# Kernel tuning notes

Hardware: AMD Instinct MI355X
Metric: run time of the kernel (lower is better)

The kernel has to match this reference:

```python
import jax, jax.numpy as jnp
import numpy as np

N = 256          # HiPPO order
DT = 1.0 / 4096  # discretization step ~ 1/L
L, BATCH = 4096, 64
GBT_ALPHA = 0.5  # bilinear transform (matches discretization=0.5)


def _legt_matrices(n):
    # Closed-form HiPPO-LegT transition matrices (Gu et al.), lambda_n=1.
    q = np.arange(n, dtype=np.float64)
    r = (2.0 * q + 1.0) ** 0.5
    j, i = np.meshgrid(q, q)  # i: row index n, j: col index k
    A = -(r[:, None] * np.where(i < j, (-1.0) ** (i - j), 1.0) * r[None, :])
    B = r[:, None]  # (N, 1)
    return A, B


def _discretize_gbt(A, B, dt, alpha):
    # Generalized bilinear transform, identical to scipy cont2discrete('gbt').
    n = A.shape[0]
    I = np.eye(n)
    M = np.linalg.inv(I - dt * alpha * A)
    dA = M @ (I + dt * (1.0 - alpha) * A)
    dB = (M @ (dt * B)).squeeze(-1)
    return dA.astype(np.float32), dB.astype(np.float32)


def setup_inputs() -> dict:
    key = jax.random.key(0)
    A, B = _legt_matrices(N)
    dA, dB = _discretize_gbt(A, B, DT, GBT_ALPHA)
    inputs = jax.random.normal(key, (L, BATCH), dtype=jnp.float32)
    return {"inputs": inputs, "dA": jnp.asarray(dA), "dB": jnp.asarray(dB)}


def reference(inputs, dA, dB):
    # inputs: (L, B); dA: (N, N); dB: (N,)
    # u_t = inputs_t[..., None] * dB  -> (L, B, N)
    u = inputs[..., None] * dB

    def step(c, u_t):
        # c_t = dA @ c_{t-1} + u_t  (row-vector form: c @ dA^T)
        c = c @ dA.T + u_t
        return c, c

    c0 = jnp.zeros(u.shape[1:], dtype=u.dtype)  # (B, N)
    _, cs = jax.lax.scan(step, c0, u)
    return cs  # (L, B, N)
```

## Files before the change

### kernel.cpp

```cpp
#include <hip/hip_runtime.h>
#include <hip/hip_bf16.h>
#include <stdint.h>


#define N 256
#define LSEQ 4096
#define BATCH 64
#define TCH 64
#define NCH 64

using bf16x8 = __attribute__((ext_vector_type(8))) __bf16;
using f32x4  = __attribute__((ext_vector_type(4))) float;

__device__ __forceinline__ unsigned short f2bf(float f) {
  uint32_t x = __builtin_bit_cast(uint32_t, f);
  uint32_t r = x + 0x7fffu + ((x >> 16) & 1u);
  return (unsigned short)(r >> 16);
}
__device__ __forceinline__ float bf2f(unsigned short h) {
  uint32_t x = ((uint32_t)h) << 16;
  return __builtin_bit_cast(float, x);
}

__device__ __forceinline__ int swz(int r, int c) { return r * 32 + ((c ^ ((r >> 1) & 3)) << 3); }

#define OFF_Phi 16777216
#define OFF_Plo 25165824
#define OFF_Kf  33554432
#define OFF_Khi 33619968
#define OFF_Klo 33652736
#define OFF_shi 33685504
#define OFF_slo 35782656
#define OFF_G0  37879808
#define OFF_uT  42074112
#define OFF_Sqh 43122688
#define OFF_Sql 43778048


__device__ __forceinline__ void mm64_tile(const float* __restrict__ A, const float* __restrict__ B,
                                          float* __restrict__ Cw, unsigned short* __restrict__ Chi,
                                          unsigned short* __restrict__ Clo, int bx, int tid,
                                          char* smem) {
  float (*At)[68] = (float(*)[68])smem;
  float (*Bs)[68] = (float(*)[68])(smem + 4352);
  int gr0 = (bx >> 2) * 64, gc0 = (bx & 3) * 64;
  int ty = tid >> 4, tx = tid & 15;
  float acc[4][4];
  #pragma unroll
  for (int r = 0; r < 4; ++r)
    #pragma unroll
    for (int c = 0; c < 4; ++c) acc[r][c] = 0.f;
  int ra = tid >> 2, ka4 = (tid & 3) << 2;
  int kb = tid >> 4, cb4 = (tid & 15) << 2;
  for (int k0 = 0; k0 < 256; k0 += 16) {
    float4 va = *(const float4*)&A[(size_t)(gr0 + ra) * 256 + k0 + ka4];
    At[ka4 + 0][ra] = va.x; At[ka4 + 1][ra] = va.y;
    At[ka4 + 2][ra] = va.z; At[ka4 + 3][ra] = va.w;
    *(float4*)&Bs[kb][cb4] = *(const float4*)&B[(size_t)(k0 + kb) * 256 + gc0 + cb4];
    __syncthreads();
    #pragma unroll
    for (int kk = 0; kk < 16; ++kk) {
      float4 a4 = *(const float4*)&At[kk][ty << 2];
      float4 b4 = *(const float4*)&Bs[kk][tx << 2];
      acc[0][0] += a4.x * b4.x; acc[0][1] += a4.x * b4.y; acc[0][2] += a4.x * b4.z; acc[0][3] += a4.x * b4.w;
      acc[1][0] += a4.y * b4.x; acc[1][1] += a4.y * b4.y; acc[1][2] += a4.y * b4.z; acc[1][3] += a4.y * b4.w;
      acc[2][0] += a4.z * b4.x; acc[2][1] += a4.z * b4.y; acc[2][2] += a4.z * b4.z; acc[2][3] += a4.z * b4.w;
      acc[3][0] += a4.w * b4.x; acc[3][1] += a4.w * b4.y; acc[3][2] += a4.w * b4.z; acc[3][3] += a4.w * b4.w;
    }
    __syncthreads();
  }
  #pragma unroll
  for (int r = 0; r < 4; ++r)
    #pragma unroll
    for (int c = 0; c < 4; ++c) {
      size_t idx = (size_t)(gr0 + ty * 4 + r) * 256 + gc0 + tx * 4 + c;
      float v = acc[r][c];
      Cw[idx] = v;
      unsigned short h = f2bf(v);
      Chi[idx] = h;
      Clo[idx] = f2bf(v - bf2f(h));
    }
}

__device__ __forceinline__ void makeK_part(const float* __restrict__ Pw, const float* __restrict__ dB,
                                           float* __restrict__ Kf, unsigned short* __restrict__ Khi,
                                           unsigned short* __restrict__ Klo, int p, int quarter, int tid) {
  if (p == 0) {
    if (quarter == 0) {
      float v = dB[tid];
      Kf[tid] = v;
      unsigned short h = f2bf(v);
      Khi[tid] = h;
      Klo[tid] = f2bf(v - bf2f(h));
    }
    return;
  }
  int lane = tid & 63, w = tid >> 6;
  const float* M = Pw + (size_t)(p - 1) * 65536;
  float d0 = dB[lane], d1 = dB[lane + 64], d2 = dB[lane + 128], d3 = dB[lane + 192];
  for (int ii = 0; ii < 16; ++ii) {
    int i = quarter * 64 + w * 16 + ii;
    const float* row = M + (size_t)i * 256;
    float acc = row[lane] * d0 + row[lane + 64] * d1 + row[lane + 128] * d2 + row[lane + 192] * d3;
    #pragma unroll
    for (int off = 32; off; off >>= 1) acc += __shfl_xor(acc, off, 64);
    if (lane == 0) {
      Kf[p * 256 + i] = acc;
      unsigned short h = f2bf(acc);
      Khi[p * 256 + i] = h;
      Klo[p * 256 + i] = f2bf(acc - bf2f(h));
    }
  }
}

__device__ __forceinline__ void finals_one(const float* __restrict__ Kf, const float* __restrict__ u,
                                           float* __restrict__ G0, int k, int b, int i) {
  float acc = 0.f;
  int ubase = (k * TCH + 63) * BATCH + b;
  #pragma unroll 8
  for (int p = 0; p < TCH; ++p)
    acc += Kf[p * N + i] * u[ubase - p * BATCH];
  G0[(size_t)(k * BATCH + b) * N + i] = acc;
}

template <int FINAL>
__device__ __forceinline__ void ks_tile(int bx, int tid, const float* __restrict__ Gin,
                                        float* __restrict__ Gout,
                                        const unsigned short* __restrict__ Mh,
                                        const unsigned short* __restrict__ Ml, int shift,
                                        unsigned short* __restrict__ shi,
                                        unsigned short* __restrict__ slo, char* smem) {
  unsigned short* Ah = (unsigned short*)smem;
  unsigned short* Al = (unsigned short*)(smem + 4096);
  unsigned short* Bh = (unsigned short*)(smem + 8192);
  unsigned short* Bl = (unsigned short*)(smem + 12288);
  int kb0 = (bx >> 2) * 64, i0 = (bx & 3) * 64;
  int lane = tid & 63, wid = tid >> 6;
  int wr = wid >> 1, wc = wid & 1;
  int rg = lane >> 4, cl = lane & 15;

  f32x4 acc[2][2];
  #pragma unroll
  for (int mf = 0; mf < 2; ++mf) {
    int m0 = kb0 + wr * 32 + mf * 16 + rg * 4;
    #pragma unroll
    for (int nf = 0; nf < 2; ++nf) {
      int i = i0 + wc * 32 + nf * 16 + cl;
      #pragma unroll
      for (int r = 0; r < 4; ++r)
        acc[mf][nf][r] = Gin[(size_t)(m0 + r) * 256 + i];
    }
  }

  int sr = tid >> 2, kc = tid & 3;
  int sw = swz(sr, kc);
  for (int kt = 0; kt < 8; ++kt) {
    int srow = kb0 + sr - shift;
    if (srow >= 0) {
      const float* src = &Gin[(size_t)srow * 256 + kt * 32 + kc * 8];
      float4 v0 = *(const float4*)src;
      float4 v1 = *(const float4*)(src + 4);
      float vv[8] = {v0.x, v0.y, v0.z, v0.w, v1.x, v1.y, v1.z, v1.w};
      unsigned short hv[8], lv[8];
      #pragma unroll
      for (int e = 0; e < 8; ++e) {
        hv[e] = f2bf(vv[e]);
        lv[e] = f2bf(vv[e] - bf2f(hv[e]));
      }
      *(uint4*)&Ah[sw] = *(const uint4*)hv;
      *(uint4*)&Al[sw] = *(const uint4*)lv;
    } else {
      uint4 z = {0, 0, 0, 0};
      *(uint4*)&Ah[sw] = z;
      *(uint4*)&Al[sw] = z;
    }
    *(uint4*)&Bh[sw] = *(const uint4*)&Mh[(size_t)(i0 + sr) * 256 + kt * 32 + kc * 8];
    *(uint4*)&Bl[sw] = *(const uint4*)&Ml[(size_t)(i0 + sr) * 256 + kt * 32 + kc * 8];
    __syncthreads();

    int fr = lane & 15, kseg = lane >> 4;
    bf16x8 ah[2], al[2], bh[2], bl[2];
    #pragma unroll
    for (int mf = 0; mf < 2; ++mf) {
      int row = wr * 32 + mf * 16 + fr;
      ah[mf] = *(const bf16x8*)&Ah[swz(row, kseg)];
      al[mf] = *(const bf16x8*)&Al[swz(row, kseg)];
    }
    #pragma unroll
    for (int nf = 0; nf < 2; ++nf) {
      int row = wc * 32 + nf * 16 + fr;
      bh[nf] = *(const bf16x8*)&Bh[swz(row, kseg)];
      bl[nf] = *(const bf16x8*)&Bl[swz(row, kseg)];
    }
    #pragma unroll
    for (int mf = 0; mf < 2; ++mf)
      #pragma unroll
      for (int nf = 0; nf < 2; ++nf) {
        acc[mf][nf] = __builtin_amdgcn_mfma_f32_16x16x32_bf16(ah[mf], bh[nf], acc[mf][nf], 0, 0, 0);
        acc[mf][nf] = __builtin_amdgcn_mfma_f32_16x16x32_bf16(ah[mf], bl[nf], acc[mf][nf], 0, 0, 0);
        acc[mf][nf] = __builtin_amdgcn_mfma_f32_16x16x32_bf16(al[mf], bh[nf], acc[mf][nf], 0, 0, 0);
      }
    __syncthreads();
  }

  #pragma unroll
  for (int mf = 0; mf < 2; ++mf) {
    int m0 = kb0 + wr * 32 + mf * 16 + rg * 4;
    #pragma unroll
    for (int nf = 0; nf < 2; ++nf) {
      int i = i0 + wc * 32 + nf * 16 + cl;
      #pragma unroll
      for (int r = 0; r < 4; ++r) {
        if (FINAL) {
          int tm = m0 + r + 64;
          if (tm < 4096) {
            float v = acc[mf][nf][r];
            unsigned short h = f2bf(v);
            shi[(size_t)tm * 256 + i] = h;
            slo[(size_t)tm * 256 + i] = f2bf(v - bf2f(h));
          }
        } else {
          Gout[(size_t)(m0 + r) * 256 + i] = acc[mf][nf][r];
        }
      }
    }
  }
  if (FINAL && kb0 == 0) {
    for (int e = tid; e < 4096; e += 256) {
      size_t o = (size_t)(e >> 6) * 256 + i0 + (e & 63);
      shi[o] = 0;
      slo[o] = 0;
    }
  }
}


__global__ __launch_bounds__(256) void prep0(const float* __restrict__ u, const float* __restrict__ dA,
                                             float* __restrict__ uT, float* __restrict__ Pw,
                                             unsigned short* __restrict__ Phi, unsigned short* __restrict__ Plo) {
  __shared__ float tile[64][65];
  int bid = blockIdx.x, tid = threadIdx.x;
  if (bid < 64) {
    int t0 = bid * 64;
    #pragma unroll
    for (int q = 0; q < 16; ++q) {
      int e = q * 256 + tid;
      int tt = e >> 6, b = e & 63;
      tile[b][tt] = u[(size_t)(t0 + tt) * 64 + b];
    }
    __syncthreads();
    #pragma unroll
    for (int q = 0; q < 16; ++q) {
      int e = q * 256 + tid;
      int b = e >> 6, tt = e & 63;
      uT[(size_t)b * 4096 + t0 + tt] = tile[b][tt];
    }
  } else {
    int base = (bid - 64) * 1024 + tid * 4;
    float4 v = *(const float4*)&dA[base];
    *(float4*)&Pw[base] = v;
    float vv[4] = {v.x, v.y, v.z, v.w};
    #pragma unroll
    for (int q = 0; q < 4; ++q) {
      unsigned short h = f2bf(vv[q]);
      Phi[base + q] = h;
      Plo[base + q] = f2bf(vv[q] - bf2f(h));
    }
  }
}

__global__ __launch_bounds__(256) void pow_level(float* __restrict__ Pw, unsigned short* __restrict__ Phi,
                                                 unsigned short* __restrict__ Plo, int half) {
  __shared__ __align__(16) char smem[16640];
  int q = blockIdx.y + 1;
  mm64_tile(Pw + (size_t)(q - 1) * 65536, Pw + (size_t)(half - 1) * 65536,
            Pw + (size_t)(half + q - 1) * 65536, Phi + (size_t)(half + q - 1) * 65536,
            Plo + (size_t)(half + q - 1) * 65536, blockIdx.x, threadIdx.x, smem);
}

__global__ __launch_bounds__(256) void make_K(const float* __restrict__ Pw, const float* __restrict__ dB,
                                              float* __restrict__ Kf, unsigned short* __restrict__ Khi,
                                              unsigned short* __restrict__ Klo) {
  makeK_part(Pw, dB, Kf, Khi, Klo, blockIdx.x >> 2, blockIdx.x & 3, threadIdx.x);
}

__global__ __launch_bounds__(256) void finals_sq(const float* __restrict__ Kf, const float* __restrict__ u,
                                                 float* __restrict__ G0,
                                                 const float* __restrict__ S0, float* __restrict__ S1,
                                                 unsigned short* __restrict__ Sqh0,
                                                 unsigned short* __restrict__ Sql0) {
  __shared__ __align__(16) char smem[16640];
  if (blockIdx.x < 64) {
    finals_one(Kf, u, G0, blockIdx.x, blockIdx.y, threadIdx.x);
  } else if (blockIdx.y < 16) {
    mm64_tile(S0, S0, S1, Sqh0, Sql0, blockIdx.y, threadIdx.x, smem);
  }
}

template <int FINAL>
__global__ __launch_bounds__(256) void ks_level(const float* __restrict__ Gin, float* __restrict__ Gout,
                                                const unsigned short* __restrict__ Mh,
                                                const unsigned short* __restrict__ Ml, int shift,
                                                unsigned short* __restrict__ shi,
                                                unsigned short* __restrict__ slo,
                                                const float* __restrict__ SqA, float* __restrict__ SqC,
                                                unsigned short* __restrict__ SqChi,
                                                unsigned short* __restrict__ SqClo) {
  __shared__ __align__(16) char smem[16640];
  int bx = blockIdx.x;
  if (bx < 256) {
    ks_tile<FINAL>(bx, threadIdx.x, Gin, Gout, Mh, Ml, shift, shi, slo, smem);
  } else {
    mm64_tile(SqA, SqA, SqC, SqChi, SqClo, bx - 256, threadIdx.x, smem);
  }
}

__global__ __launch_bounds__(256, 2) void main_gemm(const unsigned short* __restrict__ shi,
                                                    const unsigned short* __restrict__ slo,
                                                    const unsigned short* __restrict__ Phi,
                                                    const unsigned short* __restrict__ Plo,
                                                    const unsigned short* __restrict__ Khi,
                                                    const unsigned short* __restrict__ Klo,
                                                    const float* __restrict__ uT,
                                                    float* __restrict__ out) {
  __shared__ unsigned short Ah[128 * 40], Al[128 * 40], Bh[128 * 40], Bl[128 * 40];
  int dt = blockIdx.y;
  int x = blockIdx.x;
  int it = x >> 5, kbt = x & 31;
  int kb0 = kbt * 128, i0 = it * 128;
  int tid = threadIdx.x;
  int lane = tid & 63, wid = tid >> 6;
  int wr = wid >> 1, wc = wid & 1;

  f32x4 acc[4][4];
  #pragma unroll
  for (int mf = 0; mf < 4; ++mf)
    #pragma unroll
    for (int nf = 0; nf < 4; ++nf)
      #pragma unroll
      for (int r = 0; r < 4; ++r) acc[mf][nf][r] = 0.f;

  const unsigned short* PhiD = Phi + (size_t)dt * 65536;
  const unsigned short* PloD = Plo + (size_t)dt * 65536;
  int nkt = (dt >= 32) ? 10 : 9;

  for (int kt = 0; kt < nkt; ++kt) {
    int r = tid >> 1, h = tid & 1;
    if (kt < 8) {
      int co = kt * 32 + h * 16;
      const unsigned short* p1 = shi + (size_t)(kb0 + r) * 256 + co;
      const unsigned short* p2 = slo + (size_t)(kb0 + r) * 256 + co;
      const unsigned short* p3 = PhiD + (size_t)(i0 + r) * 256 + co;
      const unsigned short* p4 = PloD + (size_t)(i0 + r) * 256 + co;
      int lo_ = r * 40 + h * 16;
      *(uint4*)&Ah[lo_]     = *(const uint4*)p1;
      *(uint4*)&Ah[lo_ + 8] = *(const uint4*)(p1 + 8);
      *(uint4*)&Al[lo_]     = *(const uint4*)p2;
      *(uint4*)&Al[lo_ + 8] = *(const uint4*)(p2 + 8);
      *(uint4*)&Bh[lo_]     = *(const uint4*)p3;
      *(uint4*)&Bh[lo_ + 8] = *(const uint4*)(p3 + 8);
      *(uint4*)&Bl[lo_]     = *(const uint4*)p4;
      *(uint4*)&Bl[lo_ + 8] = *(const uint4*)(p4 + 8);
    } else {
      int p0 = (kt - 8) * 32;
      int kk = (kb0 + r) >> 6, b = (kb0 + r) & 63;
      const float* ub2 = uT + (size_t)b * 4096 + kk * 64 + dt;
      #pragma unroll
      for (int qq = 0; qq < 16; ++qq) {
        int pp = h * 16 + qq;
        int sh = p0 + pp;
        float v = (sh <= dt) ? ub2[-sh] : 0.f;
        unsigned short hv = f2bf(v);
        Ah[r * 40 + pp] = hv;
        Al[r * 40 + pp] = f2bf(v - bf2f(hv));
      }
      int n = tid & 127, ph = tid >> 7;
      #pragma unroll
      for (int qq = 0; qq < 16; ++qq) {
        int pp = ph * 16 + qq;
        Bh[n * 40 + pp] = Khi[(p0 + pp) * 256 + i0 + n];
        Bl[n * 40 + pp] = Klo[(p0 + pp) * 256 + i0 + n];
      }
    }
    __syncthreads();

    int kseg = lane >> 4, fr = lane & 15;
    bf16x8 ah[4], al[4], bh[4], bl[4];
    #pragma unroll
    for (int mf = 0; mf < 4; ++mf) {
      int row = (wr * 64 + mf * 16 + fr) * 40 + kseg * 8;
      ah[mf] = *(const bf16x8*)&Ah[row];
      al[mf] = *(const bf16x8*)&Al[row];
    }
    #pragma unroll
    for (int nf = 0; nf < 4; ++nf) {
      int row = (wc * 64 + nf * 16 + fr) * 40 + kseg * 8;
      bh[nf] = *(const bf16x8*)&Bh[row];
      bl[nf] = *(const bf16x8*)&Bl[row];
    }
    #pragma unroll
    for (int mf = 0; mf < 4; ++mf)
      #pragma unroll
      for (int nf = 0; nf < 4; ++nf) {
        acc[mf][nf] = __builtin_amdgcn_mfma_f32_16x16x32_bf16(ah[mf], bh[nf], acc[mf][nf], 0, 0, 0);
        acc[mf][nf] = __builtin_amdgcn_mfma_f32_16x16x32_bf16(ah[mf], bl[nf], acc[mf][nf], 0, 0, 0);
        acc[mf][nf] = __builtin_amdgcn_mfma_f32_16x16x32_bf16(al[mf], bh[nf], acc[mf][nf], 0, 0, 0);
      }
    __syncthreads();
  }

  int rg = lane >> 4, cl = lane & 15;
  #pragma unroll
  for (int mf = 0; mf < 4; ++mf) {
    int kbrow_base = kb0 + wr * 64 + mf * 16 + rg * 4;
    #pragma unroll
    for (int nf = 0; nf < 4; ++nf) {
      int i = i0 + wc * 64 + nf * 16 + cl;
      #pragma unroll
      for (int r = 0; r < 4; ++r) {
        int kbrow = kbrow_base + r;
        int k = kbrow >> 6, b = kbrow & 63;
        size_t t = (size_t)(k * 64 + dt);
        out[(t * 64 + b) * 256 + i] = acc[mf][nf][r];
      }
    }
  }
}


extern "C" void kernel_launch(void* const* d_in, const int* in_sizes, int n_in,
                              void* d_out, int out_size, void* d_ws, size_t ws_size,
                              hipStream_t stream) {
  (void)in_sizes; (void)n_in; (void)out_size;
  const float* u  = (const float*)d_in[0];
  const float* dA = (const float*)d_in[1];
  const float* dB = (const float*)d_in[2];
  float* out = (float*)d_out;
  char* ws = (char*)d_ws;

  float*          Pw  = (float*)(ws);
  unsigned short* Phi = (unsigned short*)(ws + OFF_Phi);
  unsigned short* Plo = (unsigned short*)(ws + OFF_Plo);
  float*          Kf  = (float*)(ws + OFF_Kf);
  unsigned short* Khi = (unsigned short*)(ws + OFF_Khi);
  unsigned short* Klo = (unsigned short*)(ws + OFF_Klo);
  unsigned short* shi = (unsigned short*)(ws + OFF_shi);
  unsigned short* slo = (unsigned short*)(ws + OFF_slo);
  float*          G0  = (float*)(ws + OFF_G0);
  unsigned short* Sqh = (unsigned short*)(ws + OFF_Sqh);
  unsigned short* Sql = (unsigned short*)(ws + OFF_Sql);

  const size_t NEED_KS = 44433408;
  if (ws_size < NEED_KS) return;

  float* G1 = (float*)ws;

  float* S[6];
  S[0] = Pw + (size_t)63 * 65536;
  for (int d = 1; d <= 5; ++d) S[d] = Pw + (size_t)(55 + d) * 65536;

  prep0<<<128, 256, 0, stream>>>(u, dA, (float*)(ws + OFF_uT), Pw, Phi, Plo);
  for (int half = 1; half <= 32; half <<= 1)
    pow_level<<<dim3(16, half), 256, 0, stream>>>(Pw, Phi, Plo, half);
  make_K<<<256, 256, 0, stream>>>(Pw, dB, Kf, Khi, Klo);

  finals_sq<<<dim3(65, 64), 256, 0, stream>>>(Kf, u, G0, S[0], S[1], Sqh, Sql);

  const unsigned short* Mh0 = Phi + (size_t)63 * 65536;
  const unsigned short* Ml0 = Plo + (size_t)63 * 65536;
  ks_level<0><<<272, 256, 0, stream>>>(G0, G1, Mh0, Ml0, 64, nullptr, nullptr,
                                       S[1], S[2], Sqh + 1 * 65536, Sql + 1 * 65536);
  ks_level<0><<<272, 256, 0, stream>>>(G1, G0, Sqh + 0 * 65536, Sql + 0 * 65536, 128, nullptr, nullptr,
                                       S[2], S[3], Sqh + 2 * 65536, Sql + 2 * 65536);
  ks_level<0><<<272, 256, 0, stream>>>(G0, G1, Sqh + 1 * 65536, Sql + 1 * 65536, 256, nullptr, nullptr,
                                       S[3], S[4], Sqh + 3 * 65536, Sql + 3 * 65536);
  ks_level<0><<<272, 256, 0, stream>>>(G1, G0, Sqh + 2 * 65536, Sql + 2 * 65536, 512, nullptr, nullptr,
                                       S[4], S[5], Sqh + 4 * 65536, Sql + 4 * 65536);
  ks_level<0><<<256, 256, 0, stream>>>(G0, G1, Sqh + 3 * 65536, Sql + 3 * 65536, 1024, nullptr, nullptr,
                                       nullptr, nullptr, nullptr, nullptr);
  ks_level<1><<<256, 256, 0, stream>>>(G1, nullptr, Sqh + 4 * 65536, Sql + 4 * 65536, 2048, shi, slo,
                                       nullptr, nullptr, nullptr, nullptr);

  main_gemm<<<dim3(64, 64), 256, 0, stream>>>(shi, slo, Phi, Plo, Khi, Klo,
                                              (const float*)(ws + OFF_uT), out);
}
```

Baseline: 376.3 us.

## Register-prefetch GEMM tiles and fuse K-vector construction into power-doubling kernels

Both the fp32 SIMT matmul tile and the split-bf16 MFMA tile now load the next k-slice from global memory into registers while the current slice is being computed, hiding load latency behind math. The separate make_K launch is removed. K vectors are built incrementally during each power-doubling level (K[half+j] = P^half · K[j]) in extra blocks of the same launch, and K[0]=dB is written in an extra prep0 block. This cuts one launch and overlaps K work with the matrix powers, at the cost of more register pressure and of extra blocks per level. The K rows now come from a chained product rather than from each power applied to dB, which can change rounding slightly.

```diff
diff --git a/kernel.cpp b/kernel.cpp
--- a/kernel.cpp
+++ b/kernel.cpp
@@ -52,12 +52,19 @@
     for (int c = 0; c < 4; ++c) acc[r][c] = 0.f;
   int ra = tid >> 2, ka4 = (tid & 3) << 2;
   int kb = tid >> 4, cb4 = (tid & 15) << 2;
+  const float* pa = &A[(size_t)(gr0 + ra) * 256 + ka4];
+  const float* pb = &B[(size_t)kb * 256 + gc0 + cb4];
+  float4 va = *(const float4*)pa;
+  float4 vb = *(const float4*)pb;
   for (int k0 = 0; k0 < 256; k0 += 16) {
-    float4 va = *(const float4*)&A[(size_t)(gr0 + ra) * 256 + k0 + ka4];
     At[ka4 + 0][ra] = va.x; At[ka4 + 1][ra] = va.y;
     At[ka4 + 2][ra] = va.z; At[ka4 + 3][ra] = va.w;
-    *(float4*)&Bs[kb][cb4] = *(const float4*)&B[(size_t)(k0 + kb) * 256 + gc0 + cb4];
-    __syncthreads();
+    *(float4*)&Bs[kb][cb4] = vb;
+    __syncthreads();
+    if (k0 + 16 < 256) {
+      va = *(const float4*)(pa + k0 + 16);
+      vb = *(const float4*)(pb + (size_t)(k0 + 16) * 256);
+    }
     #pragma unroll
     for (int kk = 0; kk < 16; ++kk) {
       float4 a4 = *(const float4*)&At[kk][ty << 2];
@@ -80,37 +87,6 @@
       Chi[idx] = h;
       Clo[idx] = f2bf(v - bf2f(h));
     }
-}
-
-__device__ __forceinline__ void makeK_part(const float* __restrict__ Pw, const float* __restrict__ dB,
-                                           float* __restrict__ Kf, unsigned short* __restrict__ Khi,
-                                           unsigned short* __restrict__ Klo, int p, int quarter, int tid) {
-  if (p == 0) {
-    if (quarter == 0) {
-      float v = dB[tid];
-      Kf[tid] = v;
-      unsigned short h = f2bf(v);
-      Khi[tid] = h;
-      Klo[tid] = f2bf(v - bf2f(h));
-    }
-    return;
-  }
-  int lane = tid & 63, w = tid >> 6;
-  const float* M = Pw + (size_t)(p - 1) * 65536;
-  float d0 = dB[lane], d1 = dB[lane + 64], d2 = dB[lane + 128], d3 = dB[lane + 192];
-  for (int ii = 0; ii < 16; ++ii) {
-    int i = quarter * 64 + w * 16 + ii;
-    const float* row = M + (size_t)i * 256;
-    float acc = row[lane] * d0 + row[lane + 64] * d1 + row[lane + 128] * d2 + row[lane + 192] * d3;
-    #pragma unroll
-    for (int off = 32; off; off >>= 1) acc += __shfl_xor(acc, off, 64);
-    if (lane == 0) {
-      Kf[p * 256 + i] = acc;
-      unsigned short h = f2bf(acc);
-      Khi[p * 256 + i] = h;
-      Klo[p * 256 + i] = f2bf(acc - bf2f(h));
-    }
-  }
 }
 
 __device__ __forceinline__ void finals_one(const float* __restrict__ Kf, const float* __restrict__ u,
@@ -154,13 +130,19 @@
 
   int sr = tid >> 2, kc = tid & 3;
   int sw = swz(sr, kc);
+  int srow = kb0 + sr - shift;
+  bool haveA = (srow >= 0);
+  const float* srcA = &Gin[(size_t)(haveA ? srow : 0) * 256 + kc * 8];
+  const unsigned short* srcBh = &Mh[(size_t)(i0 + sr) * 256 + kc * 8];
+  const unsigned short* srcBl = &Ml[(size_t)(i0 + sr) * 256 + kc * 8];
+
+  float4 rA0, rA1;
+  uint4 rBh = *(const uint4*)srcBh, rBl = *(const uint4*)srcBl;
+  if (haveA) { rA0 = *(const float4*)srcA; rA1 = *(const float4*)(srcA + 4); }
+
   for (int kt = 0; kt < 8; ++kt) {
-    int srow = kb0 + sr - shift;
-    if (srow >= 0) {
-      const float* src = &Gin[(size_t)srow * 256 + kt * 32 + kc * 8];
-      float4 v0 = *(const float4*)src;
-      float4 v1 = *(const float4*)(src + 4);
-      float vv[8] = {v0.x, v0.y, v0.z, v0.w, v1.x, v1.y, v1.z, v1.w};
+    if (haveA) {
+      float vv[8] = {rA0.x, rA0.y, rA0.z, rA0.w, rA1.x, rA1.y, rA1.z, rA1.w};
       unsigned short hv[8], lv[8];
       #pragma unroll
       for (int e = 0; e < 8; ++e) {
@@ -174,9 +156,16 @@
       *(uint4*)&Ah[sw] = z;
       *(uint4*)&Al[sw] = z;
     }
-    *(uint4*)&Bh[sw] = *(const uint4*)&Mh[(size_t)(i0 + sr) * 256 + kt * 32 + kc * 8];
-    *(uint4*)&Bl[sw] = *(const uint4*)&Ml[(size_t)(i0 + sr) * 256 + kt * 32 + kc * 8];
-    __syncthreads();
+    *(uint4*)&Bh[sw] = rBh;
+    *(uint4*)&Bl[sw] = rBl;
+    __syncthreads();
+
+    if (kt < 7) {
+      int off = (kt + 1) * 32;
+      if (haveA) { rA0 = *(const float4*)(srcA + off); rA1 = *(const float4*)(srcA + off + 4); }
+      rBh = *(const uint4*)(srcBh + off);
+      rBl = *(const uint4*)(srcBl + off);
+    }
 
     int fr = lane & 15, kseg = lane >> 4;
     bf16x8 ah[2], al[2], bh[2], bl[2];
@@ -236,8 +225,11 @@
 
 
 __global__ __launch_bounds__(256) void prep0(const float* __restrict__ u, const float* __restrict__ dA,
+                                             const float* __restrict__ dB,
                                              float* __restrict__ uT, float* __restrict__ Pw,
-                                             unsigned short* __restrict__ Phi, unsigned short* __restrict__ Plo) {
+                                             unsigned short* __restrict__ Phi, unsigned short* __restrict__ Plo,
+                                             float* __restrict__ Kf, unsigned short* __restrict__ Khi,
+                                             unsigned short* __restrict__ Klo) {
   __shared__ float tile[64][65];
   int bid = blockIdx.x, tid = threadIdx.x;
   if (bid < 64) {
@@ -255,7 +247,7 @@
       int b = e >> 6, tt = e & 63;
       uT[(size_t)b * 4096 + t0 + tt] = tile[b][tt];
     }
-  } else {
+  } else if (bid < 128) {
     int base = (bid - 64) * 1024 + tid * 4;
     float4 v = *(const float4*)&dA[base];
     *(float4*)&Pw[base] = v;
@@ -266,22 +258,51 @@
       Phi[base + q] = h;
       Plo[base + q] = f2bf(vv[q] - bf2f(h));
     }
-  }
-}
-
-__global__ __launch_bounds__(256) void pow_level(float* __restrict__ Pw, unsigned short* __restrict__ Phi,
-                                                 unsigned short* __restrict__ Plo, int half) {
+  } else {
+    float v = dB[tid];
+    Kf[tid] = v;
+    unsigned short h = f2bf(v);
+    Khi[tid] = h;
+    Klo[tid] = f2bf(v - bf2f(h));
+  }
+}
+
+__global__ __launch_bounds__(256) void pow_K(float* __restrict__ Pw,
+                                             unsigned short* __restrict__ Phi,
+                                             unsigned short* __restrict__ Plo,
+                                             float* __restrict__ Kf,
+                                             unsigned short* __restrict__ Khi,
+                                             unsigned short* __restrict__ Klo,
+                                             int half) {
   __shared__ __align__(16) char smem[16640];
-  int q = blockIdx.y + 1;
-  mm64_tile(Pw + (size_t)(q - 1) * 65536, Pw + (size_t)(half - 1) * 65536,
-            Pw + (size_t)(half + q - 1) * 65536, Phi + (size_t)(half + q - 1) * 65536,
-            Plo + (size_t)(half + q - 1) * 65536, blockIdx.x, threadIdx.x, smem);
-}
-
-__global__ __launch_bounds__(256) void make_K(const float* __restrict__ Pw, const float* __restrict__ dB,
-                                              float* __restrict__ Kf, unsigned short* __restrict__ Khi,
-                                              unsigned short* __restrict__ Klo) {
-  makeK_part(Pw, dB, Kf, Khi, Klo, blockIdx.x >> 2, blockIdx.x & 3, threadIdx.x);
+  int bx = blockIdx.x, tid = threadIdx.x;
+  if (bx < 16 * half) {
+    int q = (bx >> 4) + 1, t = bx & 15;
+    mm64_tile(Pw + (size_t)(q - 1) * 65536, Pw + (size_t)(half - 1) * 65536,
+              Pw + (size_t)(half + q - 1) * 65536, Phi + (size_t)(half + q - 1) * 65536,
+              Plo + (size_t)(half + q - 1) * 65536, t, tid, smem);
+  } else {
+    int r = bx - 16 * half;
+    int jp = r >> 2, quarter = r & 3;
+    int p = half + jp;
+    const float* M = Pw + (size_t)(half - 1) * 65536;
+    const float* v = Kf + (size_t)jp * 256;
+    int lane = tid & 63, w = tid >> 6;
+    float d0 = v[lane], d1 = v[lane + 64], d2 = v[lane + 128], d3 = v[lane + 192];
+    for (int ii = 0; ii < 16; ++ii) {
+      int i = quarter * 64 + w * 16 + ii;
+      const float* row = M + (size_t)i * 256;
+      float acc = row[lane] * d0 + row[lane + 64] * d1 + row[lane + 128] * d2 + row[lane + 192] * d3;
+      #pragma unroll
+      for (int off = 32; off; off >>= 1) acc += __shfl_xor(acc, off, 64);
+      if (lane == 0) {
+        Kf[p * 256 + i] = acc;
+        unsigned short h = f2bf(acc);
+        Khi[p * 256 + i] = h;
+        Klo[p * 256 + i] = f2bf(acc - bf2f(h));
+      }
+    }
+  }
 }
 
 __global__ __launch_bounds__(256) void finals_sq(const float* __restrict__ Kf, const float* __restrict__ u,
@@ -459,10 +480,9 @@
   S[0] = Pw + (size_t)63 * 65536;
   for (int d = 1; d <= 5; ++d) S[d] = Pw + (size_t)(55 + d) * 65536;
 
-  prep0<<<128, 256, 0, stream>>>(u, dA, (float*)(ws + OFF_uT), Pw, Phi, Plo);
+  prep0<<<129, 256, 0, stream>>>(u, dA, dB, (float*)(ws + OFF_uT), Pw, Phi, Plo, Kf, Khi, Klo);
   for (int half = 1; half <= 32; half <<= 1)
-    pow_level<<<dim3(16, half), 256, 0, stream>>>(Pw, Phi, Plo, half);
-  make_K<<<256, 256, 0, stream>>>(Pw, dB, Kf, Khi, Klo);
+    pow_K<<<20 * half, 256, 0, stream>>>(Pw, Phi, Plo, Kf, Khi, Klo, half);
 
   finals_sq<<<dim3(65, 64), 256, 0, stream>>>(Kf, u, G0, S[0], S[1], Sqh, Sql);
 
```

New measurement: 341.5 us. -9.3%, faster.
